# Optimization experiments

Measured on AMD Instinct MI355X. Metric: run time of the kernel, lower is better.

Reference implementation:

```python
import jax, jax.numpy as jnp
import numpy as np
from jax import lax

B, CI, CO, H, W, K, RANK, SR = 8, 64, 64, 256, 256, 3, 4, 1
SHIFTS = [(dy, dx) for dy in range(-SR, SR + 1) for dx in range(-SR, SR + 1)]  # 9 shifts
N_PAIRS = len(SHIFTS) * (len(SHIFTS) + 1) // 2  # 45 unordered pairs (j >= i)


def conv3x3(x, w, b):
    # torch Conv2d == cross-correlation, 'SAME' padding for odd kernel
    y = lax.conv_general_dilated(x, w, window_strides=(1, 1), padding='SAME',
                                 dimension_numbers=('NCHW', 'OIHW', 'NCHW'))
    return y + b[None, :, None, None]


def setup_inputs() -> dict:
    key = jax.random.key(0)
    ks = jax.random.split(key, 7)
    return {
        'x': jax.random.normal(ks[0], (B, CI, H, W), jnp.float32) * 0.5,
        'linear_w': jax.random.normal(ks[1], (CO, CI, K, K), jnp.float32) * 0.05,
        'linear_b': jax.random.normal(ks[2], (CO,), jnp.float32) * 0.05,
        'w2a_w': jax.random.normal(ks[3], (RANK, CO, CI), jnp.float32) * 0.05,
        'w2a_b': jax.random.normal(ks[4], (RANK, CO), jnp.float32) * 0.05,
        'w2b_w': jax.random.normal(ks[5], (RANK, CO, CO), jnp.float32) * 0.05,
        'w2b_b': jax.random.normal(ks[6], (RANK, CO), jnp.float32) * 0.05,
    }


def reference(x, linear_w, linear_b, w2a_w, w2a_b, w2b_w, w2b_b):
    # Linear Volterra term: 3x3 conv
    F1 = conv3x3(x, linear_w, linear_b)

    # Quadratic term. Original loops over 45 shift pairs (i <= j) computing
    # prod = Xi*Xj and pushing each through the rank-q 1x1 convs. Since the
    # 1x1 convs are affine, (1/P) * sum_pairs Wb(Wa(prod)) == Wb(Wa(S/P))
    # where S = sum_{i<=j} Xi*Xj. And S = ((sum_i Xi)^2 + sum_i Xi^2) / 2.
    sum_x = jnp.zeros_like(x)
    sum_x2 = jnp.zeros_like(x)
    x2 = x * x
    for (dy, dx) in SHIFTS:  # fixed structural loop over 9 circular shifts
        sum_x = sum_x + jnp.roll(x, (dy, dx), axis=(2, 3))
        sum_x2 = sum_x2 + jnp.roll(x2, (dy, dx), axis=(2, 3))
    S = 0.5 * (sum_x * sum_x + sum_x2)  # [B, CI, H, W]
    Sn = S / N_PAIRS

    F2 = jnp.zeros_like(F1)
    for q in range(RANK):  # fixed small rank loop
        h = jnp.einsum('oi,bihw->bohw', w2a_w[q], Sn) + w2a_b[q][None, :, None, None]
        F2 = F2 + jnp.einsum('oi,bihw->bohw', w2b_w[q], h) + w2b_b[q][None, :, None, None]

    return F1 + F2
```

## Files before the change

kernel.cpp:

```cpp
#include <hip/hip_runtime.h>

#define NB 8
#define NC 64
#define NH 256
#define NW 256

typedef short s16x8 __attribute__((ext_vector_type(8)));
typedef float f32x16 __attribute__((ext_vector_type(16)));

static __device__ __forceinline__ unsigned short f2bf(float f) {
  unsigned int u = __float_as_uint(f);
  unsigned int r = (u + 0x7fffu + ((u >> 16) & 1u)) >> 16;
  return (unsigned short)r;
}

#define WS_NEEDED 134299904ull
#define CKSTRIDE 16777216ull

static __device__ __forceinline__ int wfoff(int tap, int co, int ci) {
  int ck = ci >> 4;
  int lane = (((ci >> 3) & 1) << 5) | (co & 31);
  int m = co >> 5;
  return ((((ck * 10 + tap) * 2 + m) * 64 + lane) << 3) | (ci & 7);
}

__global__ __launch_bounds__(256) void prep_fast(
    const float* __restrict__ lw, const float* __restrict__ lb,
    const float* __restrict__ w2a_w, const float* __restrict__ w2a_b,
    const float* __restrict__ w2b_w, const float* __restrict__ w2b_b,
    unsigned short* __restrict__ Wf, float* __restrict__ bias) {
  int blk = blockIdx.x;
  int t = threadIdx.x;
  if (blk < 16) {
    int gidx = blk * 256 + t;
    int ci = gidx & 63, co = gidx >> 6;
    float acc = 0.f;
    for (int q = 0; q < 4; ++q) {
      const float* wb = w2b_w + (q * 64 + co) * 64;
      const float* wa = w2a_w + q * 4096 + ci;
      for (int c = 0; c < 64; ++c) acc += wb[c] * wa[c * 64];
    }
    Wf[wfoff(9, co, ci)] = f2bf(acc * (1.0f / 90.0f));
    return;
  }
  for (int idx = (blk - 16) * 256 + t; idx < 64 * 64 * 9; idx += 48 * 256) {
    int ci = idx & 63;
    int co = (idx >> 6) & 63;
    int tap = idx >> 12;
    Wf[wfoff(tap, co, ci)] = f2bf(lw[(co * 64 + ci) * 9 + tap]);
  }
  if (blk == 16 && t < 64) {
    float acc = lb[t];
    for (int q = 0; q < 4; ++q) {
      const float* wb = w2b_w + (q * 64 + t) * 64;
      const float* ba = w2a_b + q * 64;
      for (int c = 0; c < 64; ++c) acc += wb[c] * ba[c];
      acc += w2b_b[q * 64 + t];
    }
    bias[t] = acc;
  }
}

__global__ __launch_bounds__(512, 4) void stage1(
    const float* __restrict__ x, unsigned short* __restrict__ xT,
    unsigned short* __restrict__ snT) {
  __shared__ __align__(16) unsigned short xb[NW * 64];
  __shared__ __align__(16) unsigned short sb[NW * 64];
  int id = blockIdx.x;
  int bid = (id & 7) * 256 + (id >> 3);
  int b = bid >> 8, h = bid & 255;
  int tid = threadIdx.x;
  int w = tid & 255;
  int ciBase = (tid >> 8) * 32;
  int hm = (h + 255) & 255, hp = (h + 1) & 255;
  int wm = (w + 255) & 255, wp = (w + 1) & 255;
  const float* xbase = x + (size_t)b * 64 * 65536;
  char* xbc = (char*)xb;
  char* sbc = (char*)sb;
  int swz = (w & 7) << 4;
  int rowm = hm * 256, row0 = h * 256, rowp = hp * 256;
  for (int i = 0; i < 16; ++i) {
    int ci = ciBase + i * 2;
    const float* p0 = xbase + (size_t)ci * 65536;
    const float* p1 = p0 + 65536;
    float a0 = p0[rowm + wm], a1 = p0[rowm + w], a2 = p0[rowm + wp];
    float b0 = p0[row0 + wm], b1 = p0[row0 + w], b2 = p0[row0 + wp];
    float c0 = p0[rowp + wm], c1 = p0[rowp + w], c2 = p0[rowp + wp];
    float d0 = p1[rowm + wm], d1 = p1[rowm + w], d2 = p1[rowm + wp];
    float e0 = p1[row0 + wm], e1 = p1[row0 + w], e2 = p1[row0 + wp];
    float f0 = p1[rowp + wm], f1 = p1[rowp + w], f2 = p1[rowp + wp];
    float u0 = a0 + a1 + a2 + b0 + b1 + b2 + c0 + c1 + c2;
    float v0 = a0 * a0 + a1 * a1 + a2 * a2 + b0 * b0 + b1 * b1 + b2 * b2 +
               c0 * c0 + c1 * c1 + c2 * c2;
    float u1 = d0 + d1 + d2 + e0 + e1 + e2 + f0 + f1 + f2;
    float v1 = d0 * d0 + d1 * d1 + d2 * d2 + e0 * e0 + e1 * e1 + e2 * e2 +
               f0 * f0 + f1 * f1 + f2 * f2;
    float sn0 = u0 * u0 + v0;
    float sn1 = u1 * u1 + v1;
    unsigned int xp = (unsigned int)f2bf(b1) | ((unsigned int)f2bf(e1) << 16);
    unsigned int sp = (unsigned int)f2bf(sn0) | ((unsigned int)f2bf(sn1) << 16);
    int off = (w * 128 + ci * 2) ^ swz;
    *(unsigned int*)(xbc + off) = xp;
    *(unsigned int*)(sbc + off) = sp;
  }
  __syncthreads();
  int r = tid >> 3, c = tid & 7;
  int ck = c >> 1, half = c & 1;
  size_t pbase = (size_t)b * 65536 + (size_t)h * 256;
  char* xdst = (char*)xT + (size_t)ck * CKSTRIDE + half * 16;
  char* sdst = (char*)snT + (size_t)ck * CKSTRIDE + half * 16;
#pragma unroll
  for (int pass = 0; pass < 4; ++pass) {
    int rr = r + pass * 64;
    int loff = (rr * 128 + c * 16) ^ ((rr & 7) << 4);
    float4 vx = *(float4*)(xbc + loff);
    float4 vs = *(float4*)(sbc + loff);
    *(float4*)(xdst + (pbase + rr) * 32) = vx;
    *(float4*)(sdst + (pbase + rr) * 32) = vs;
  }
}

#define XH_OFF 0
#define SN_OFF 19008
#define WL_OFF 31296
#define LDS_SZ 51776

__global__ __launch_bounds__(256, 3) void stage2(
    const unsigned short* __restrict__ xT, const unsigned short* __restrict__ snT,
    const unsigned short* __restrict__ Wf, const float* __restrict__ bias,
    float* __restrict__ out) {
  __shared__ __align__(16) char smem[LDS_SZ];
  int id = blockIdx.x;
  int bid = (id & 7) * 256 + (id >> 3);
  int b = bid >> 8;
  int rem = bid & 255;
  int h0 = (rem >> 2) * 4, w0 = (rem & 3) * 64;
  int tid = threadIdx.x;
  int lane = tid & 63, wv = tid >> 6;
  int l31 = lane & 31, g = lane >> 5;

  f32x16 acc[2][2];
#pragma unroll
  for (int m = 0; m < 2; ++m)
#pragma unroll
    for (int n = 0; n < 2; ++n)
#pragma unroll
      for (int i = 0; i < 16; ++i) acc[m][n][i] = 0.f;

  for (int ck = 0; ck < 4; ++ck) {
    const char* xsrc = (const char*)xT + (size_t)ck * CKSTRIDE;
    const char* ssrc = (const char*)snT + (size_t)ck * CKSTRIDE;
    const char* wsrc = (const char*)Wf + ck * 20480;
    __syncthreads();
    for (int idx = tid; idx < 792; idx += 256) {
      int row = idx >> 1, half = idx & 1;
      int hr = row / 66, wc = row - hr * 66;
      int gh = h0 - 1 + hr, gw = w0 - 1 + wc;
      float4 v = make_float4(0.f, 0.f, 0.f, 0.f);
      if ((unsigned)gh < 256u && (unsigned)gw < 256u)
        v = *(const float4*)(xsrc +
              ((size_t)b * 65536 + gh * 256 + gw) * 32 + half * 16);
      *(float4*)(smem + XH_OFF + row * 48 + half * 16) = v;
    }
    for (int idx = tid; idx < 512; idx += 256) {
      int row = idx >> 1, half = idx & 1;
      int ph = row >> 6, pw = row & 63;
      float4 v = *(const float4*)(ssrc +
            ((size_t)b * 65536 + (h0 + ph) * 256 + w0 + pw) * 32 + half * 16);
      *(float4*)(smem + SN_OFF + row * 48 + half * 16) = v;
    }
    for (int idx = tid; idx < 1280; idx += 256) {
      float4 v = *(const float4*)(wsrc + idx * 16);
      *(float4*)(smem + WL_OFF + idx * 16) = v;
    }
    __syncthreads();

#pragma unroll
    for (int s = 0; s < 10; ++s) {
      s16x8 af[2], bf[2];
#pragma unroll
      for (int m = 0; m < 2; ++m)
        af[m] = *(const s16x8*)(smem + WL_OFF + ((s * 2 + m) * 64 + lane) * 16);
      if (s < 9) {
        const int dy = s / 3, dx = s - dy * 3;
        int rbase = ((wv + dy) * 66 + l31 + dx) * 48 + g * 16;
#pragma unroll
        for (int n = 0; n < 2; ++n)
          bf[n] = *(const s16x8*)(smem + XH_OFF + rbase + n * 32 * 48);
      } else {
        int rbase = (wv * 64 + l31) * 48 + g * 16;
#pragma unroll
        for (int n = 0; n < 2; ++n)
          bf[n] = *(const s16x8*)(smem + SN_OFF + rbase + n * 32 * 48);
      }
#pragma unroll
      for (int m = 0; m < 2; ++m)
#pragma unroll
        for (int n = 0; n < 2; ++n)
          acc[m][n] = __builtin_amdgcn_mfma_f32_32x32x16_bf16(af[m], bf[n],
                                                              acc[m][n], 0, 0, 0);
    }
  }

  int h = h0 + wv;
#pragma unroll
  for (int m = 0; m < 2; ++m) {
#pragma unroll
    for (int reg = 0; reg < 16; ++reg) {
      int co = m * 32 + (reg & 3) + 8 * (reg >> 2) + 4 * (lane >> 5);
      float bv = bias[co];
#pragma unroll
      for (int n = 0; n < 2; ++n) {
        int w = w0 + n * 32 + l31;
        out[(((size_t)b * 64 + co) * 256 + h) * 256 + w] = acc[m][n][reg] + bv;
      }
    }
  }
}

#define TW 128
#define CC 16

__global__ __launch_bounds__(256) void prep_kernel(
    const float* __restrict__ lw, const float* __restrict__ w2a_w,
    const float* __restrict__ w2a_b, const float* __restrict__ w2b_w,
    const float* __restrict__ w2b_b, float* __restrict__ Mt,
    float* __restrict__ bias2, float* __restrict__ Wt) {
  int t = threadIdx.x;
  for (int idx = t; idx < NC * NC; idx += 256) {
    int i = idx >> 6, o = idx & 63;
    float acc = 0.f;
    for (int q = 0; q < 4; ++q) {
      const float* wb = w2b_w + (q * NC + o) * NC;
      const float* wa = w2a_w + q * NC * NC + i;
      for (int c = 0; c < NC; ++c) acc += wb[c] * wa[c * NC];
    }
    Mt[idx] = acc;
  }
  if (t < NC) {
    float acc = 0.f;
    for (int q = 0; q < 4; ++q) {
      const float* wb = w2b_w + (q * NC + t) * NC;
      const float* ba = w2a_b + q * NC;
      for (int c = 0; c < NC; ++c) acc += wb[c] * ba[c];
      acc += w2b_b[q * NC + t];
    }
    bias2[t] = acc;
  }
  for (int idx = t; idx < NC * 9 * NC; idx += 256) {
    int co = idx & 63;
    int tap = (idx >> 6) % 9;
    int ci = idx / (9 * 64);
    Wt[idx] = lw[(co * NC + ci) * 9 + tap];
  }
}

__global__ __launch_bounds__(256) void volterra_main(
    const float* __restrict__ x, const float* __restrict__ lb,
    const float* __restrict__ Mt, const float* __restrict__ bias2,
    const float* __restrict__ Wt, float* __restrict__ out) {
  __shared__ __align__(16) float xt[CC][3][TW + 8];
  __shared__ __align__(16) float snt[CC][TW];
  const int tid = threadIdx.x;
  const int wc = blockIdx.x;
  const int h = blockIdx.y;
  const int b = blockIdx.z;
  const int w0 = wc * TW;
  const int co = tid >> 2;
  const int wq = tid & 3;
  const int wl0 = wq * 32;
  const bool fix_lo = (w0 == 0) && (wq == 0);
  const bool fix_hi = (w0 + TW == NW) && (wq == 3);
  float acc[32];
  {
    float base = lb[co] + bias2[co];
#pragma unroll
    for (int k = 0; k < 32; ++k) acc[k] = base;
  }
  for (int cc = 0; cc < NC / CC; ++cc) {
    const int ci0 = cc * CC;
    __syncthreads();
    for (int idx = tid; idx < CC * 3 * (TW + 2); idx += 256) {
      int col = idx % (TW + 2);
      int rem = idx / (TW + 2);
      int dy = rem % 3;
      int ci = rem / 3;
      int gr = (h + dy - 1 + NH) & (NH - 1);
      int gc = (w0 - 1 + col + NW) & (NW - 1);
      xt[ci][dy][col] = x[(((size_t)b * NC + ci0 + ci) * NH + gr) * NW + gc];
    }
    __syncthreads();
    for (int idx = tid; idx < CC * TW; idx += 256) {
      int ci = idx >> 7, wl = idx & (TW - 1);
      float s1 = 0.f, s2 = 0.f;
#pragma unroll
      for (int dy = 0; dy < 3; ++dy)
#pragma unroll
        for (int dx = 0; dx < 3; ++dx) {
          float v = xt[ci][dy][wl + dx];
          s1 += v;
          s2 += v * v;
        }
      snt[ci][wl] = (s1 * s1 + s2) * (0.5f / 45.0f);
    }
    __syncthreads();
    for (int ci = 0; ci < CC; ++ci) {
      const int cig = ci0 + ci;
      {
        float m = Mt[cig * NC + co];
        const float4* sp = reinterpret_cast<const float4*>(&snt[ci][wl0]);
#pragma unroll
        for (int j = 0; j < 8; ++j) {
          float4 v = sp[j];
          acc[4 * j + 0] += m * v.x;
          acc[4 * j + 1] += m * v.y;
          acc[4 * j + 2] += m * v.z;
          acc[4 * j + 3] += m * v.w;
        }
      }
      const float* wtp = Wt + cig * 9 * NC + co;
#pragma unroll
      for (int dy = 0; dy < 3; ++dy) {
        if (dy == 0 && h == 0) continue;
        if (dy == 2 && h == NH - 1) continue;
        float wv0 = wtp[(dy * 3 + 0) * NC];
        float wv1 = wtp[(dy * 3 + 1) * NC];
        float wv2 = wtp[(dy * 3 + 2) * NC];
        float xr[34];
        const float4* rp = reinterpret_cast<const float4*>(&xt[ci][dy][wl0]);
#pragma unroll
        for (int j = 0; j < 8; ++j) {
          float4 v = rp[j];
          xr[4 * j + 0] = v.x;
          xr[4 * j + 1] = v.y;
          xr[4 * j + 2] = v.z;
          xr[4 * j + 3] = v.w;
        }
        xr[32] = xt[ci][dy][wl0 + 32];
        xr[33] = xt[ci][dy][wl0 + 33];
        if (fix_lo) xr[0] = 0.f;
        if (fix_hi) xr[33] = 0.f;
#pragma unroll
        for (int k = 0; k < 32; ++k) {
          acc[k] += wv0 * xr[k] + wv1 * xr[k + 1] + wv2 * xr[k + 2];
        }
      }
    }
  }
  float* op = out + (((size_t)b * NC + co) * NH + h) * NW + w0 + wl0;
#pragma unroll
  for (int j = 0; j < 8; ++j) {
    float4 v;
    v.x = acc[4 * j + 0];
    v.y = acc[4 * j + 1];
    v.z = acc[4 * j + 2];
    v.w = acc[4 * j + 3];
    reinterpret_cast<float4*>(op)[j] = v;
  }
}

extern "C" void kernel_launch(void* const* d_in, const int* in_sizes, int n_in,
                              void* d_out, int out_size, void* d_ws, size_t ws_size,
                              hipStream_t stream) {
  const float* x = (const float*)d_in[0];
  const float* lw = (const float*)d_in[1];
  const float* lb = (const float*)d_in[2];
  const float* w2a_w = (const float*)d_in[3];
  const float* w2a_b = (const float*)d_in[4];
  const float* w2b_w = (const float*)d_in[5];
  const float* w2b_b = (const float*)d_in[6];
  float* out = (float*)d_out;

  if (ws_size >= WS_NEEDED) {
    char* ws = (char*)d_ws;
    unsigned short* xT = (unsigned short*)(ws);
    unsigned short* snT = (unsigned short*)(ws + 67108864);
    unsigned short* Wf = (unsigned short*)(ws + 134217728);
    float* bias = (float*)(ws + 134299648);
    prep_fast<<<64, 256, 0, stream>>>(lw, lb, w2a_w, w2a_b, w2b_w, w2b_b, Wf, bias);
    stage1<<<2048, 512, 0, stream>>>(x, xT, snT);
    stage2<<<2048, 256, 0, stream>>>(xT, snT, Wf, bias, out);
  } else {
    float* ws = (float*)d_ws;
    float* Mt = ws;
    float* bias2 = ws + 4096;
    float* Wt = ws + 4096 + 64;
    prep_kernel<<<1, 256, 0, stream>>>(lw, w2a_w, w2a_b, w2b_w, w2b_b, Mt, bias2, Wt);
    dim3 grid(NW / TW, NH, NB);
    volterra_main<<<grid, 256, 0, stream>>>(x, lb, Mt, bias2, Wt, out);
  }
}
```

Baseline: 365.9 us.

## Fuse bf16 transpose and quadratic-sum prologue into conv/MFMA kernel

Removes the separate stage1 kernel that wrote channel-interleaved bf16 copies of x and the squared-shift sum to a large workspace. Each stage2 block now loads its fp32 x halo tile (16 channels, 6x66) straight into LDS, builds the bf16 x tile and the 3x3 sum-of-squares term from it, then runs the MFMA loop. This drops the global round trip of the intermediates and one launch, at the cost of more LDS per block (occupancy hint lowered from 3 to 2), scalar strided global loads, and redundant halo reads.

```diff
diff --git a/kernel.cpp b/kernel.cpp
--- a/kernel.cpp
+++ b/kernel.cpp
@@ -14,8 +14,7 @@
   return (unsigned short)r;
 }
 
-#define WS_NEEDED 134299904ull
-#define CKSTRIDE 16777216ull
+#define WS_NEEDED 82176ull
 
 static __device__ __forceinline__ int wfoff(int tap, int co, int ci) {
   int ck = ci >> 4;
@@ -61,74 +60,15 @@
   }
 }
 
-__global__ __launch_bounds__(512, 4) void stage1(
-    const float* __restrict__ x, unsigned short* __restrict__ xT,
-    unsigned short* __restrict__ snT) {
-  __shared__ __align__(16) unsigned short xb[NW * 64];
-  __shared__ __align__(16) unsigned short sb[NW * 64];
-  int id = blockIdx.x;
-  int bid = (id & 7) * 256 + (id >> 3);
-  int b = bid >> 8, h = bid & 255;
-  int tid = threadIdx.x;
-  int w = tid & 255;
-  int ciBase = (tid >> 8) * 32;
-  int hm = (h + 255) & 255, hp = (h + 1) & 255;
-  int wm = (w + 255) & 255, wp = (w + 1) & 255;
-  const float* xbase = x + (size_t)b * 64 * 65536;
-  char* xbc = (char*)xb;
-  char* sbc = (char*)sb;
-  int swz = (w & 7) << 4;
-  int rowm = hm * 256, row0 = h * 256, rowp = hp * 256;
-  for (int i = 0; i < 16; ++i) {
-    int ci = ciBase + i * 2;
-    const float* p0 = xbase + (size_t)ci * 65536;
-    const float* p1 = p0 + 65536;
-    float a0 = p0[rowm + wm], a1 = p0[rowm + w], a2 = p0[rowm + wp];
-    float b0 = p0[row0 + wm], b1 = p0[row0 + w], b2 = p0[row0 + wp];
-    float c0 = p0[rowp + wm], c1 = p0[rowp + w], c2 = p0[rowp + wp];
-    float d0 = p1[rowm + wm], d1 = p1[rowm + w], d2 = p1[rowm + wp];
-    float e0 = p1[row0 + wm], e1 = p1[row0 + w], e2 = p1[row0 + wp];
-    float f0 = p1[rowp + wm], f1 = p1[rowp + w], f2 = p1[rowp + wp];
-    float u0 = a0 + a1 + a2 + b0 + b1 + b2 + c0 + c1 + c2;
-    float v0 = a0 * a0 + a1 * a1 + a2 * a2 + b0 * b0 + b1 * b1 + b2 * b2 +
-               c0 * c0 + c1 * c1 + c2 * c2;
-    float u1 = d0 + d1 + d2 + e0 + e1 + e2 + f0 + f1 + f2;
-    float v1 = d0 * d0 + d1 * d1 + d2 * d2 + e0 * e0 + e1 * e1 + e2 * e2 +
-               f0 * f0 + f1 * f1 + f2 * f2;
-    float sn0 = u0 * u0 + v0;
-    float sn1 = u1 * u1 + v1;
-    unsigned int xp = (unsigned int)f2bf(b1) | ((unsigned int)f2bf(e1) << 16);
-    unsigned int sp = (unsigned int)f2bf(sn0) | ((unsigned int)f2bf(sn1) << 16);
-    int off = (w * 128 + ci * 2) ^ swz;
-    *(unsigned int*)(xbc + off) = xp;
-    *(unsigned int*)(sbc + off) = sp;
-  }
-  __syncthreads();
-  int r = tid >> 3, c = tid & 7;
-  int ck = c >> 1, half = c & 1;
-  size_t pbase = (size_t)b * 65536 + (size_t)h * 256;
-  char* xdst = (char*)xT + (size_t)ck * CKSTRIDE + half * 16;
-  char* sdst = (char*)snT + (size_t)ck * CKSTRIDE + half * 16;
-#pragma unroll
-  for (int pass = 0; pass < 4; ++pass) {
-    int rr = r + pass * 64;
-    int loff = (rr * 128 + c * 16) ^ ((rr & 7) << 4);
-    float4 vx = *(float4*)(xbc + loff);
-    float4 vs = *(float4*)(sbc + loff);
-    *(float4*)(xdst + (pbase + rr) * 32) = vx;
-    *(float4*)(sdst + (pbase + rr) * 32) = vs;
-  }
-}
-
-#define XH_OFF 0
-#define SN_OFF 19008
-#define WL_OFF 31296
-#define LDS_SZ 51776
-
-__global__ __launch_bounds__(256, 3) void stage2(
-    const unsigned short* __restrict__ xT, const unsigned short* __restrict__ snT,
-    const unsigned short* __restrict__ Wf, const float* __restrict__ bias,
-    float* __restrict__ out) {
+#define XF_OFF 0
+#define XH_OFF 26112
+#define SN_OFF 45120
+#define WL_OFF 57408
+#define LDS_SZ 77888
+
+__global__ __launch_bounds__(256, 2) void stage2(
+    const float* __restrict__ x, const unsigned short* __restrict__ Wf,
+    const float* __restrict__ bias, float* __restrict__ out) {
   __shared__ __align__(16) char smem[LDS_SZ];
   int id = blockIdx.x;
   int bid = (id & 7) * 256 + (id >> 3);
@@ -148,30 +88,66 @@
       for (int i = 0; i < 16; ++i) acc[m][n][i] = 0.f;
 
   for (int ck = 0; ck < 4; ++ck) {
-    const char* xsrc = (const char*)xT + (size_t)ck * CKSTRIDE;
-    const char* ssrc = (const char*)snT + (size_t)ck * CKSTRIDE;
-    const char* wsrc = (const char*)Wf + ck * 20480;
+    int ci0 = ck * 16;
+    for (int idx = tid; idx < 6336; idx += 256) {
+      int wc = idx % 66;
+      int t2 = idx / 66;
+      int hr = t2 % 6;
+      int ci = t2 / 6;
+      int gh = (h0 - 1 + hr) & 255;
+      int gw = (w0 - 1 + wc) & 255;
+      float v = x[(((size_t)b * 64 + ci0 + ci) * 256 + gh) * 256 + gw];
+      *(float*)(smem + XF_OFF + ((ci * 6 + hr) * 68 + wc) * 4) = v;
+    }
     __syncthreads();
     for (int idx = tid; idx < 792; idx += 256) {
       int row = idx >> 1, half = idx & 1;
       int hr = row / 66, wc = row - hr * 66;
       int gh = h0 - 1 + hr, gw = w0 - 1 + wc;
-      float4 v = make_float4(0.f, 0.f, 0.f, 0.f);
-      if ((unsigned)gh < 256u && (unsigned)gw < 256u)
-        v = *(const float4*)(xsrc +
-              ((size_t)b * 65536 + gh * 256 + gw) * 32 + half * 16);
-      *(float4*)(smem + XH_OFF + row * 48 + half * 16) = v;
+      uint4 pk = make_uint4(0u, 0u, 0u, 0u);
+      if ((unsigned)gh < 256u && (unsigned)gw < 256u) {
+        const char* base = smem + XF_OFF + (hr * 68 + wc) * 4;
+        unsigned int* pp = (unsigned int*)&pk;
+#pragma unroll
+        for (int j = 0; j < 4; ++j) {
+          int cl = half * 8 + 2 * j;
+          float lo = *(const float*)(base + (cl) * 6 * 68 * 4);
+          float hi = *(const float*)(base + (cl + 1) * 6 * 68 * 4);
+          pp[j] = (unsigned int)f2bf(lo) | ((unsigned int)f2bf(hi) << 16);
+        }
+      }
+      *(uint4*)(smem + XH_OFF + row * 48 + half * 16) = pk;
     }
     for (int idx = tid; idx < 512; idx += 256) {
       int row = idx >> 1, half = idx & 1;
       int ph = row >> 6, pw = row & 63;
-      float4 v = *(const float4*)(ssrc +
-            ((size_t)b * 65536 + (h0 + ph) * 256 + w0 + pw) * 32 + half * 16);
-      *(float4*)(smem + SN_OFF + row * 48 + half * 16) = v;
-    }
-    for (int idx = tid; idx < 1280; idx += 256) {
-      float4 v = *(const float4*)(wsrc + idx * 16);
-      *(float4*)(smem + WL_OFF + idx * 16) = v;
+      uint4 pk;
+      unsigned int* pp = (unsigned int*)&pk;
+#pragma unroll
+      for (int j = 0; j < 4; ++j) {
+        unsigned int two = 0;
+#pragma unroll
+        for (int e = 0; e < 2; ++e) {
+          int cl = half * 8 + 2 * j + e;
+          const float* p = (const float*)(smem + XF_OFF) + (cl * 6 + ph) * 68 + pw;
+          float u = p[0] + p[1] + p[2] + p[68] + p[69] + p[70] +
+                    p[136] + p[137] + p[138];
+          float v = p[0]*p[0] + p[1]*p[1] + p[2]*p[2] +
+                    p[68]*p[68] + p[69]*p[69] + p[70]*p[70] +
+                    p[136]*p[136] + p[137]*p[137] + p[138]*p[138];
+          float sn = u * u + v;
+          two |= ((unsigned int)f2bf(sn)) << (16 * e);
+        }
+        pp[j] = two;
+      }
+      *(uint4*)(smem + SN_OFF + row * 48 + half * 16) = pk;
+    }
+    {
+      const char* wsrc = (const char*)Wf + ck * 20480;
+      for (int idx = tid; idx < 1280; idx += 256) {
+        float4 v = *(const float4*)(wsrc + idx * 16);
+        *(float4*)(smem + WL_OFF + idx * 16) = v;
+      }
     }
     __syncthreads();
 
@@ -373,13 +349,10 @@
 
   if (ws_size >= WS_NEEDED) {
     char* ws = (char*)d_ws;
-    unsigned short* xT = (unsigned short*)(ws);
-    unsigned short* snT = (unsigned short*)(ws + 67108864);
-    unsigned short* Wf = (unsigned short*)(ws + 134217728);
-    float* bias = (float*)(ws + 134299648);
+    unsigned short* Wf = (unsigned short*)(ws);
+    float* bias = (float*)(ws + 81920);
     prep_fast<<<64, 256, 0, stream>>>(lw, lb, w2a_w, w2a_b, w2b_w, w2b_b, Wf, bias);
-    stage1<<<2048, 512, 0, stream>>>(x, xT, snT);
-    stage2<<<2048, 256, 0, stream>>>(xT, snT, Wf, bias, out);
+    stage2<<<2048, 256, 0, stream>>>(x, Wf, bias, out);
   } else {
     float* ws = (float*)d_ws;
     float* Mt = ws;
```

After: 377.6 us. 3.2% more time.
